# Performance work log

Hardware: AMD Instinct MI355X
Metric: run time of the kernel (lower is better)

Reference implementation:

```python
import jax, jax.numpy as jnp
import numpy as np

SAMPLE_RATE = 44100.0
MIN_GAIN, MAX_GAIN = -12.0, 12.0
MIN_Q, MAX_Q = 0.1, 10.0
# (min, max) for the 15 normalized control params, in channel order
PARAM_RANGES = np.array([
    (MIN_GAIN, MAX_GAIN), (20.0, 2000.0), (MIN_Q, MAX_Q),      # low shelf
    (MIN_GAIN, MAX_GAIN), (20.0, 200.0), (MIN_Q, MAX_Q),       # band0 peaking
    (MIN_GAIN, MAX_GAIN), (200.0, 2000.0), (MIN_Q, MAX_Q),     # band1 peaking
    (MIN_GAIN, MAX_GAIN), (2000.0, 12000.0), (MIN_Q, MAX_Q),   # band2 peaking
    (MIN_GAIN, MAX_GAIN), (4000.0, 16000.0), (MIN_Q, MAX_Q),   # high shelf
], dtype=np.float32)


def _biquad(gain_db, f0, q, ftype):
    """RBJ cookbook biquad. Inputs shape (bs,), returns (bs, 6) normalized so a0==1."""
    A = 10.0 ** (gain_db / 40.0)
    w0 = 2.0 * jnp.pi * (f0 / SAMPLE_RATE)
    alpha = jnp.sin(w0) / (2.0 * q)
    cw = jnp.cos(w0)
    sA = jnp.sqrt(A)
    if ftype == 'peaking':
        b0 = 1.0 + alpha * A; b1 = -2.0 * cw; b2 = 1.0 - alpha * A
        a0 = 1.0 + alpha / A; a1 = -2.0 * cw; a2 = 1.0 - alpha / A
    elif ftype == 'low_shelf':
        b0 = A * ((A + 1) - (A - 1) * cw + 2 * sA * alpha)
        b1 = 2 * A * ((A - 1) - (A + 1) * cw)
        b2 = A * ((A + 1) - (A - 1) * cw - 2 * sA * alpha)
        a0 = (A + 1) + (A - 1) * cw + 2 * sA * alpha
        a1 = -2 * ((A - 1) + (A + 1) * cw)
        a2 = (A + 1) + (A - 1) * cw - 2 * sA * alpha
    else:  # high_shelf
        b0 = A * ((A + 1) + (A - 1) * cw + 2 * sA * alpha)
        b1 = -2 * A * ((A - 1) + (A + 1) * cw)
        b2 = A * ((A + 1) + (A - 1) * cw - 2 * sA * alpha)
        a0 = (A + 1) - (A - 1) * cw + 2 * sA * alpha
        a1 = 2 * ((A - 1) - (A + 1) * cw)
        a2 = (A + 1) - (A - 1) * cw - 2 * sA * alpha
    coeffs = jnp.stack([b0, b1, b2, a0, a1, a2], axis=-1)
    return coeffs / a0[..., None]


def _compute_sos(p):
    """p: (bs, 15) denormalized params -> sos (bs, 5, 6)."""
    secs = [
        _biquad(p[:, 0], p[:, 1], p[:, 2], 'low_shelf'),
        _biquad(p[:, 3], p[:, 4], p[:, 5], 'peaking'),
        _biquad(p[:, 6], p[:, 7], p[:, 8], 'peaking'),
        _biquad(p[:, 9], p[:, 10], p[:, 11], 'peaking'),
        _biquad(p[:, 12], p[:, 13], p[:, 14], 'high_shelf'),
    ]
    return jnp.stack(secs, axis=1)


def _sosfilt(sos, x):
    """Cascaded 5-section biquad, direct form II transposed, zero initial state.
    sos: (bs, 5, 6), x: (bs, T) -> (bs, T)."""
    b0, b1, b2 = sos[..., 0], sos[..., 1], sos[..., 2]  # each (bs, 5)
    a1, a2 = sos[..., 4], sos[..., 5]

    def step(carry, xt):
        z1, z2 = carry  # (bs, 5) each
        s = xt  # (bs,)
        z1n, z2n = [], []
        for k in range(5):  # fixed small cascade
            y = b0[:, k] * s + z1[:, k]
            z1n.append(b1[:, k] * s - a1[:, k] * y + z2[:, k])
            z2n.append(b2[:, k] * s - a2[:, k] * y)
            s = y
        return (jnp.stack(z1n, 1), jnp.stack(z2n, 1)), s

    bs = x.shape[0]
    z0 = jnp.zeros((bs, 5), x.dtype)
    _, y = jax.lax.scan(step, (z0, z0), x.T)
    return y.T


def setup_inputs() -> dict:
    key = jax.random.key(0)
    k1, k2 = jax.random.split(key)
    x = jax.random.normal(k1, (32, 1, 131072), dtype=jnp.float32)
    control_params = jax.random.uniform(k2, (32, 15, 1), dtype=jnp.float32)
    return {"x": x, "control_params": control_params}


def reference(x, control_params):
    # denormalize: min + p * (max - min)
    lo = jnp.asarray(PARAM_RANGES[:, 0])
    hi = jnp.asarray(PARAM_RANGES[:, 1])
    p = control_params[:, :, 0]  # (bs, 15)
    p_denorm = lo[None, :] + p * (hi - lo)[None, :]
    sos = _compute_sos(p_denorm)           # (bs, 5, 6)
    y = _sosfilt(sos, x[:, 0, :])          # (bs, T)
    return y[:, None, :], sos
```

## Files before the change

kernel.cpp:

```cpp
#include <hip/hip_runtime.h>
#include <math.h>


#define NB 32
#define LCH 32
#define T_LEN 131072
#define C_CH (T_LEN / LCH)
#define SPANS (C_CH / 64)
#define NPOW 12

__constant__ double c_lo[15] = {-12.0,   20.0, 0.1,
                                -12.0,   20.0, 0.1,
                                -12.0,  200.0, 0.1,
                                -12.0, 2000.0, 0.1,
                                -12.0, 4000.0, 0.1};
__constant__ double c_hi[15] = { 12.0,  2000.0, 10.0,
                                 12.0,   200.0, 10.0,
                                 12.0,  2000.0, 10.0,
                                 12.0, 12000.0, 10.0,
                                 12.0, 16000.0, 10.0};

__global__ __launch_bounds__(128)
void eq_setup(const float* __restrict__ cp, float* __restrict__ sos_out,
              float* __restrict__ powers)
{
    int b = blockIdx.x;
    int t = threadIdx.x;
    __shared__ float  sc[5][5];
    __shared__ double Abuf[2][10][10];

    if (t < 5) {
        int k = t;
        double p[3];
#pragma unroll
        for (int j = 0; j < 3; ++j) {
            int i = k * 3 + j;
            double pv = (double)cp[b * 15 + i];
            p[j] = c_lo[i] + pv * (c_hi[i] - c_lo[i]);
        }
        double A     = exp(p[0] * (M_LN10 / 40.0));
        double w0    = 2.0 * M_PI * p[1] / 44100.0;
        double alpha = sin(w0) / (2.0 * p[2]);
        double cw    = cos(w0);
        double sA    = sqrt(A);
        double b0, b1, b2, a0, a1, a2;
        if (k == 0) {
            b0 =     A * ((A + 1) - (A - 1) * cw + 2 * sA * alpha);
            b1 = 2 * A * ((A - 1) - (A + 1) * cw);
            b2 =     A * ((A + 1) - (A - 1) * cw - 2 * sA * alpha);
            a0 =          (A + 1) + (A - 1) * cw + 2 * sA * alpha;
            a1 =    -2 * ((A - 1) + (A + 1) * cw);
            a2 =          (A + 1) + (A - 1) * cw - 2 * sA * alpha;
        } else if (k == 4) {
            b0 =     A * ((A + 1) + (A - 1) * cw + 2 * sA * alpha);
            b1 = -2 * A * ((A - 1) + (A + 1) * cw);
            b2 =     A * ((A + 1) + (A - 1) * cw - 2 * sA * alpha);
            a0 =          (A + 1) - (A - 1) * cw + 2 * sA * alpha;
            a1 =     2 * ((A - 1) - (A + 1) * cw);
            a2 =          (A + 1) - (A - 1) * cw - 2 * sA * alpha;
        } else {
            b0 = 1.0 + alpha * A;
            b1 = -2.0 * cw;
            b2 = 1.0 - alpha * A;
            a0 = 1.0 + alpha / A;
            a1 = -2.0 * cw;
            a2 = 1.0 - alpha / A;
        }
        double inv = 1.0 / a0;
        float fb0 = (float)(b0 * inv), fb1 = (float)(b1 * inv), fb2 = (float)(b2 * inv);
        float fa1 = (float)(a1 * inv), fa2 = (float)(a2 * inv);
        float* o = sos_out + (size_t)(b * 5 + k) * 6;
        o[0] = fb0; o[1] = fb1; o[2] = fb2; o[3] = 1.0f; o[4] = fa1; o[5] = fa2;
        sc[k][0] = fb0; sc[k][1] = fb1; sc[k][2] = fb2; sc[k][3] = fa1; sc[k][4] = fa2;
    }
    __syncthreads();

    if (t < 10) {
        double z[10];
#pragma unroll
        for (int i = 0; i < 10; ++i) z[i] = 0.0;
        z[t] = 1.0;
        double s = 0.0;
        double zn[10];
#pragma unroll
        for (int k = 0; k < 5; ++k) {
            double b0 = sc[k][0], b1 = sc[k][1], b2 = sc[k][2];
            double a1 = sc[k][3], a2 = sc[k][4];
            double y = b0 * s + z[2 * k];
            zn[2 * k]     = b1 * s - a1 * y + z[2 * k + 1];
            zn[2 * k + 1] = b2 * s - a2 * y;
            s = y;
        }
#pragma unroll
        for (int r = 0; r < 10; ++r) Abuf[0][r][t] = zn[r];
    }
    __syncthreads();

    int r = t / 10, cc = t % 10;
    int cur = 0;
    for (int sq = 0; sq < 16; ++sq) {
        double acc = 0.0;
        if (t < 100) {
#pragma unroll
            for (int j = 0; j < 10; ++j) acc += Abuf[cur][r][j] * Abuf[cur][j][cc];
        }
        __syncthreads();
        if (t < 100) Abuf[cur ^ 1][r][cc] = acc;
        __syncthreads();
        cur ^= 1;
        if (sq >= 4 && t < 100) {
            int m = sq - 4;
            powers[((size_t)b * NPOW + m) * 100 + t] = (float)Abuf[cur][r][cc];
        }
    }
}

__device__ __forceinline__ void ks_scan(float sv[10], const float* __restrict__ Pb, int lane)
{
#pragma unroll
    for (int j = 0; j < 6; ++j) {
        const float* P = Pb + j * 100;
        float u[10];
#pragma unroll
        for (int i = 0; i < 10; ++i) u[i] = __shfl_up(sv[i], 1 << j);
        if (lane >= (1 << j)) {
            float ns[10];
#pragma unroll
            for (int rr = 0; rr < 10; ++rr) {
                float acc = sv[rr];
#pragma unroll
                for (int c2 = 0; c2 < 10; ++c2) acc = fmaf(P[rr * 10 + c2], u[c2], acc);
                ns[rr] = acc;
            }
#pragma unroll
            for (int i = 0; i < 10; ++i) sv[i] = ns[i];
        }
    }
}

__global__ __launch_bounds__(64)
void eq_pass1(const float* __restrict__ x, const float* __restrict__ sos,
              const float* __restrict__ powers,
              float* __restrict__ v, float* __restrict__ Tspan)
{
    int blk = blockIdx.x;
    int b = blk / SPANS, sp = blk % SPANS;
    int l = threadIdx.x;
    int c = sp * 64 + l;

    const float* s5 = sos + (size_t)(b * 5) * 6;
    float cb0[5], cb1[5], cb2[5], ca1[5], ca2[5];
#pragma unroll
    for (int k = 0; k < 5; ++k) {
        cb0[k] = s5[k * 6 + 0]; cb1[k] = s5[k * 6 + 1]; cb2[k] = s5[k * 6 + 2];
        ca1[k] = s5[k * 6 + 4]; ca2[k] = s5[k * 6 + 5];
    }
    float z1[5] = {0, 0, 0, 0, 0}, z2[5] = {0, 0, 0, 0, 0};

    const float* xp = x + (size_t)b * T_LEN + (size_t)c * LCH;
#pragma unroll
    for (int t0 = 0; t0 < LCH; t0 += 4) {
        float4 xv = *reinterpret_cast<const float4*>(xp + t0);
        float in4[4] = {xv.x, xv.y, xv.z, xv.w};
#pragma unroll
        for (int j = 0; j < 4; ++j) {
            float s = in4[j];
#pragma unroll
            for (int k = 0; k < 5; ++k) {
                float yk = fmaf(cb0[k], s, z1[k]);
                float u  = fmaf(cb1[k], s, z2[k]);
                z1[k] = fmaf(-ca1[k], yk, u);
                z2[k] = fmaf(-ca2[k], yk, cb2[k] * s);
                s = yk;
            }
        }
    }

    float sv[10];
#pragma unroll
    for (int k = 0; k < 5; ++k) { sv[2 * k] = z1[k]; sv[2 * k + 1] = z2[k]; }

    size_t vb = ((size_t)(b * SPANS + sp) * 10) * 64 + l;
#pragma unroll
    for (int i = 0; i < 10; ++i) v[vb + (size_t)i * 64] = sv[i];

    const float* Pb = powers + (size_t)b * NPOW * 100;
    ks_scan(sv, Pb, l);

    if (l == 63) {
#pragma unroll
        for (int i = 0; i < 10; ++i) Tspan[(size_t)(b * 10 + i) * 64 + sp] = sv[i];
    }
}

__global__ __launch_bounds__(64)
void eq_seedscan(const float* __restrict__ powers, const float* __restrict__ Tspan,
                 float* __restrict__ seeds)
{
    int b = blockIdx.x;
    int l = threadIdx.x;
    float sv[10];
#pragma unroll
    for (int i = 0; i < 10; ++i) sv[i] = Tspan[(size_t)(b * 10 + i) * 64 + l];

    const float* Pb = powers + (size_t)b * NPOW * 100 + 6 * 100;
    ks_scan(sv, Pb, l);

    float e[10];
#pragma unroll
    for (int i = 0; i < 10; ++i) e[i] = __shfl_up(sv[i], 1);
    if (l == 0) {
#pragma unroll
        for (int i = 0; i < 10; ++i) e[i] = 0.0f;
    }
#pragma unroll
    for (int i = 0; i < 10; ++i) seeds[(size_t)(b * 10 + i) * 64 + l] = e[i];
}

__global__ __launch_bounds__(64)
void eq_pass2(const float* __restrict__ x, const float* __restrict__ sos,
              const float* __restrict__ powers, const float* __restrict__ v,
              const float* __restrict__ seeds, float* __restrict__ y)
{
    int blk = blockIdx.x;
    int b = blk / SPANS, sp = blk % SPANS;
    int l = threadIdx.x;
    int c = sp * 64 + l;

    float sv[10];
    if (l == 0) {
#pragma unroll
        for (int i = 0; i < 10; ++i) sv[i] = seeds[(size_t)(b * 10 + i) * 64 + sp];
    } else {
        size_t vb = ((size_t)(b * SPANS + sp) * 10) * 64 + (l - 1);
#pragma unroll
        for (int i = 0; i < 10; ++i) sv[i] = v[vb + (size_t)i * 64];
    }

    const float* Pb = powers + (size_t)b * NPOW * 100;
    ks_scan(sv, Pb, l);

    const float* s5 = sos + (size_t)(b * 5) * 6;
    float cb0[5], cb1[5], cb2[5], ca1[5], ca2[5];
#pragma unroll
    for (int k = 0; k < 5; ++k) {
        cb0[k] = s5[k * 6 + 0]; cb1[k] = s5[k * 6 + 1]; cb2[k] = s5[k * 6 + 2];
        ca1[k] = s5[k * 6 + 4]; ca2[k] = s5[k * 6 + 5];
    }
    float z1[5], z2[5];
#pragma unroll
    for (int k = 0; k < 5; ++k) { z1[k] = sv[2 * k]; z2[k] = sv[2 * k + 1]; }

    const float* xp = x + (size_t)b * T_LEN + (size_t)c * LCH;
    float*       yp = y + (size_t)b * T_LEN + (size_t)c * LCH;
#pragma unroll
    for (int t0 = 0; t0 < LCH; t0 += 4) {
        float4 xv = *reinterpret_cast<const float4*>(xp + t0);
        float in4[4] = {xv.x, xv.y, xv.z, xv.w};
        float o4[4];
#pragma unroll
        for (int j = 0; j < 4; ++j) {
            float s = in4[j];
#pragma unroll
            for (int k = 0; k < 5; ++k) {
                float yk = fmaf(cb0[k], s, z1[k]);
                float u  = fmaf(cb1[k], s, z2[k]);
                z1[k] = fmaf(-ca1[k], yk, u);
                z2[k] = fmaf(-ca2[k], yk, cb2[k] * s);
                s = yk;
            }
            o4[j] = s;
        }
        *reinterpret_cast<float4*>(yp + t0) = make_float4(o4[0], o4[1], o4[2], o4[3]);
    }
}

extern "C" void kernel_launch(void* const* d_in, const int* in_sizes, int n_in,
                              void* d_out, int out_size, void* d_ws, size_t ws_size,
                              hipStream_t stream)
{
    const float* x  = (const float*)d_in[0];
    const float* cp = (const float*)d_in[1];
    float* out = (float*)d_out;
    float* sos = out + (size_t)NB * T_LEN;

    float* v      = (float*)d_ws;
    float* Tspan  = v + (size_t)NB * C_CH * 10;
    float* seeds  = Tspan + (size_t)NB * 10 * 64;
    float* powers = seeds + (size_t)NB * 10 * 64;

    eq_setup<<<dim3(NB), dim3(128), 0, stream>>>(cp, sos, powers);
    eq_pass1<<<dim3(NB * SPANS), dim3(64), 0, stream>>>(x, sos, powers, v, Tspan);
    eq_seedscan<<<dim3(NB), dim3(64), 0, stream>>>(powers, Tspan, seeds);
    eq_pass2<<<dim3(NB * SPANS), dim3(64), 0, stream>>>(x, sos, powers, v, seeds, out);
}
```

Measured before the change: 50.99 us.

## Fuse filter passes into one cooperative kernel with grid sync and register-held input

Merges pass1, the seed scan and pass2 into a single cooperative kernel separated by a grid-wide barrier. Each block keeps its 32-sample input chunk in registers, so x is read from global memory once. Per-chunk carries are no longer written out and rescanned; each lane reconstructs its carry from its own scan prefix plus a propagated span seed, applied through binary matrix powers. This removes two kernel launches and the round trips through the v and seeds buffers, at the cost of a grid.sync, more register pressure, and redundant per-block span scans.

```diff
diff --git a/kernel.cpp b/kernel.cpp
--- a/kernel.cpp
+++ b/kernel.cpp
@@ -1,5 +1,8 @@
 #include <hip/hip_runtime.h>
+#include <hip/hip_cooperative_groups.h>
 #include <math.h>
+
+namespace cg = cooperative_groups;
 
 
 #define NB 32
@@ -139,14 +142,14 @@
 }
 
 __global__ __launch_bounds__(64)
-void eq_pass1(const float* __restrict__ x, const float* __restrict__ sos,
-              const float* __restrict__ powers,
-              float* __restrict__ v, float* __restrict__ Tspan)
-{
+void eq_main(const float* __restrict__ x, const float* __restrict__ sos,
+             const float* __restrict__ powers, float* __restrict__ Tspan,
+             float* __restrict__ y)
+{
+    cg::grid_group grid = cg::this_grid();
     int blk = blockIdx.x;
-    int b = blk / SPANS, sp = blk % SPANS;
+    int b = blk >> 6, sp = blk & 63;
     int l = threadIdx.x;
-    int c = sp * 64 + l;
 
     const float* s5 = sos + (size_t)(b * 5) * 6;
     float cb0[5], cb1[5], cb2[5], ca1[5], ca2[5];
@@ -155,112 +158,93 @@
         cb0[k] = s5[k * 6 + 0]; cb1[k] = s5[k * 6 + 1]; cb2[k] = s5[k * 6 + 2];
         ca1[k] = s5[k * 6 + 4]; ca2[k] = s5[k * 6 + 5];
     }
-    float z1[5] = {0, 0, 0, 0, 0}, z2[5] = {0, 0, 0, 0, 0};
-
+
+    int c = sp * 64 + l;
     const float* xp = x + (size_t)b * T_LEN + (size_t)c * LCH;
+    float xr[LCH];
 #pragma unroll
     for (int t0 = 0; t0 < LCH; t0 += 4) {
         float4 xv = *reinterpret_cast<const float4*>(xp + t0);
-        float in4[4] = {xv.x, xv.y, xv.z, xv.w};
-#pragma unroll
-        for (int j = 0; j < 4; ++j) {
-            float s = in4[j];
-#pragma unroll
-            for (int k = 0; k < 5; ++k) {
-                float yk = fmaf(cb0[k], s, z1[k]);
-                float u  = fmaf(cb1[k], s, z2[k]);
-                z1[k] = fmaf(-ca1[k], yk, u);
-                z2[k] = fmaf(-ca2[k], yk, cb2[k] * s);
-                s = yk;
-            }
-        }
-    }
-
+        xr[t0] = xv.x; xr[t0 + 1] = xv.y; xr[t0 + 2] = xv.z; xr[t0 + 3] = xv.w;
+    }
+
+    float z1[5] = {0, 0, 0, 0, 0}, z2[5] = {0, 0, 0, 0, 0};
+#pragma unroll
+    for (int j = 0; j < LCH; ++j) {
+        float s = xr[j];
+#pragma unroll
+        for (int k = 0; k < 5; ++k) {
+            float yk = fmaf(cb0[k], s, z1[k]);
+            float u  = fmaf(cb1[k], s, z2[k]);
+            z1[k] = fmaf(-ca1[k], yk, u);
+            z2[k] = fmaf(-ca2[k], yk, cb2[k] * s);
+            s = yk;
+        }
+    }
     float sv[10];
 #pragma unroll
     for (int k = 0; k < 5; ++k) { sv[2 * k] = z1[k]; sv[2 * k + 1] = z2[k]; }
-
-    size_t vb = ((size_t)(b * SPANS + sp) * 10) * 64 + l;
-#pragma unroll
-    for (int i = 0; i < 10; ++i) v[vb + (size_t)i * 64] = sv[i];
 
     const float* Pb = powers + (size_t)b * NPOW * 100;
     ks_scan(sv, Pb, l);
 
+    float es[10];
+#pragma unroll
+    for (int i = 0; i < 10; ++i) es[i] = __shfl_up(sv[i], 1);
+    if (l == 0) {
+#pragma unroll
+        for (int i = 0; i < 10; ++i) es[i] = 0.0f;
+    }
+
     if (l == 63) {
 #pragma unroll
         for (int i = 0; i < 10; ++i) Tspan[(size_t)(b * 10 + i) * 64 + sp] = sv[i];
     }
-}
-
-__global__ __launch_bounds__(64)
-void eq_seedscan(const float* __restrict__ powers, const float* __restrict__ Tspan,
-                 float* __restrict__ seeds)
-{
-    int b = blockIdx.x;
-    int l = threadIdx.x;
-    float sv[10];
-#pragma unroll
-    for (int i = 0; i < 10; ++i) sv[i] = Tspan[(size_t)(b * 10 + i) * 64 + l];
-
-    const float* Pb = powers + (size_t)b * NPOW * 100 + 6 * 100;
-    ks_scan(sv, Pb, l);
-
-    float e[10];
-#pragma unroll
-    for (int i = 0; i < 10; ++i) e[i] = __shfl_up(sv[i], 1);
-    if (l == 0) {
-#pragma unroll
-        for (int i = 0; i < 10; ++i) e[i] = 0.0f;
-    }
-#pragma unroll
-    for (int i = 0; i < 10; ++i) seeds[(size_t)(b * 10 + i) * 64 + l] = e[i];
-}
-
-__global__ __launch_bounds__(64)
-void eq_pass2(const float* __restrict__ x, const float* __restrict__ sos,
-              const float* __restrict__ powers, const float* __restrict__ v,
-              const float* __restrict__ seeds, float* __restrict__ y)
-{
-    int blk = blockIdx.x;
-    int b = blk / SPANS, sp = blk % SPANS;
-    int l = threadIdx.x;
-    int c = sp * 64 + l;
-
-    float sv[10];
-    if (l == 0) {
-#pragma unroll
-        for (int i = 0; i < 10; ++i) sv[i] = seeds[(size_t)(b * 10 + i) * 64 + sp];
-    } else {
-        size_t vb = ((size_t)(b * SPANS + sp) * 10) * 64 + (l - 1);
-#pragma unroll
-        for (int i = 0; i < 10; ++i) sv[i] = v[vb + (size_t)i * 64];
-    }
-
-    const float* Pb = powers + (size_t)b * NPOW * 100;
-    ks_scan(sv, Pb, l);
-
-    const float* s5 = sos + (size_t)(b * 5) * 6;
-    float cb0[5], cb1[5], cb2[5], ca1[5], ca2[5];
+
+    grid.sync();
+
+    float tv[10];
+#pragma unroll
+    for (int i = 0; i < 10; ++i) tv[i] = Tspan[(size_t)(b * 10 + i) * 64 + l];
+    ks_scan(tv, Pb + 6 * 100, l);
+
+    float sd[10];
+#pragma unroll
+    for (int i = 0; i < 10; ++i) sd[i] = __shfl(tv[i], (sp - 1) & 63);
+    if (sp == 0) {
+#pragma unroll
+        for (int i = 0; i < 10; ++i) sd[i] = 0.0f;
+    }
+
+#pragma unroll
+    for (int m = 0; m < 6; ++m) {
+        const float* P = Pb + m * 100;
+        float ns[10];
+#pragma unroll
+        for (int rr = 0; rr < 10; ++rr) {
+            float acc = 0.0f;
+#pragma unroll
+            for (int c2 = 0; c2 < 10; ++c2) acc = fmaf(P[rr * 10 + c2], sd[c2], acc);
+            ns[rr] = acc;
+        }
+        bool on = (l >> m) & 1;
+#pragma unroll
+        for (int i = 0; i < 10; ++i) sd[i] = on ? ns[i] : sd[i];
+    }
+
 #pragma unroll
     for (int k = 0; k < 5; ++k) {
-        cb0[k] = s5[k * 6 + 0]; cb1[k] = s5[k * 6 + 1]; cb2[k] = s5[k * 6 + 2];
-        ca1[k] = s5[k * 6 + 4]; ca2[k] = s5[k * 6 + 5];
-    }
-    float z1[5], z2[5];
-#pragma unroll
-    for (int k = 0; k < 5; ++k) { z1[k] = sv[2 * k]; z2[k] = sv[2 * k + 1]; }
-
-    const float* xp = x + (size_t)b * T_LEN + (size_t)c * LCH;
-    float*       yp = y + (size_t)b * T_LEN + (size_t)c * LCH;
+        z1[k] = es[2 * k]     + sd[2 * k];
+        z2[k] = es[2 * k + 1] + sd[2 * k + 1];
+    }
+
+    float* yp = y + (size_t)b * T_LEN + (size_t)c * LCH;
 #pragma unroll
     for (int t0 = 0; t0 < LCH; t0 += 4) {
-        float4 xv = *reinterpret_cast<const float4*>(xp + t0);
-        float in4[4] = {xv.x, xv.y, xv.z, xv.w};
         float o4[4];
 #pragma unroll
         for (int j = 0; j < 4; ++j) {
-            float s = in4[j];
+            float s = xr[t0 + j];
 #pragma unroll
             for (int k = 0; k < 5; ++k) {
                 float yk = fmaf(cb0[k], s, z1[k]);
@@ -284,13 +268,14 @@
     float* out = (float*)d_out;
     float* sos = out + (size_t)NB * T_LEN;
 
-    float* v      = (float*)d_ws;
-    float* Tspan  = v + (size_t)NB * C_CH * 10;
-    float* seeds  = Tspan + (size_t)NB * 10 * 64;
-    float* powers = seeds + (size_t)NB * 10 * 64;
+    float* powers = (float*)d_ws;
+    float* Tspan  = powers + (size_t)NB * NPOW * 100;
 
     eq_setup<<<dim3(NB), dim3(128), 0, stream>>>(cp, sos, powers);
-    eq_pass1<<<dim3(NB * SPANS), dim3(64), 0, stream>>>(x, sos, powers, v, Tspan);
-    eq_seedscan<<<dim3(NB), dim3(64), 0, stream>>>(powers, Tspan, seeds);
-    eq_pass2<<<dim3(NB * SPANS), dim3(64), 0, stream>>>(x, sos, powers, v, seeds, out);
-}
+
+    const float* xs = x; const float* ss = sos; const float* ps = powers;
+    float* ts = Tspan; float* ys = out;
+    void* kargs[] = { (void*)&xs, (void*)&ss, (void*)&ps, (void*)&ts, (void*)&ys };
+    hipLaunchCooperativeKernel((void*)eq_main, dim3(NB * SPANS), dim3(64),
+                               kargs, 0, stream);
+}
```

After: 196.0 us. 3.84x slower.
